# Kernel tuning notes

Measured on AMD Instinct MI355X. Metric: run time of the kernel, lower is better.

The kernel has to match this reference:

```python
import jax, jax.numpy as jnp
import numpy as np

EPS = 1e-8  # torch nn.CosineSimilarity default eps


def setup_inputs() -> dict:
    key = jax.random.key(0)
    k1, k2 = jax.random.split(key)
    text_encodings = jax.random.normal(k1, (65536, 256), dtype=jnp.float32)
    label_encodings = jax.random.normal(k2, (1024, 256), dtype=jnp.float32)
    return {"text_encodings": text_encodings, "label_encodings": label_encodings}


def reference(text_encodings, label_encodings):
    # cosine_sim(x, y) = x.y / max(||x||*||y||, eps), computed as one matmul
    dots = jnp.einsum('nd,ld->nl', text_encodings, label_encodings)  # [N, L]
    tn = jnp.linalg.norm(text_encodings, axis=-1)    # [N]
    ln = jnp.linalg.norm(label_encodings, axis=-1)   # [L]
    denom = jnp.maximum(tn[:, None] * ln[None, :], EPS)
    return dots / denom
```

## Files before the change

### kernel.cpp

```cpp
#include <hip/hip_runtime.h>
#include <hip/hip_bf16.h>

#define NT 65536
#define NL 1024
#define DD 256

#define BM 128
#define BN 128
#define BK 64
#define TPB 16

typedef __attribute__((ext_vector_type(4))) float f32x4;
typedef __attribute__((ext_vector_type(8))) short bf16x8;

__device__ inline short f2bf(float x) {
    union { __hip_bfloat16 b; short s; } u;
    u.b = __float2bfloat16(x);
    return u.s;
}

__device__ inline void gload_lds16(const void* g, void* l) {
    __builtin_amdgcn_global_load_lds((const __attribute__((address_space(1))) void*)g,
                                     (__attribute__((address_space(3))) void*)l,
                                     16, 0, 0);
}

__global__ __launch_bounds__(256) void prep_k(const float* __restrict__ A,
                                              const float* __restrict__ Bm,
                                              short* __restrict__ Abf,
                                              short* __restrict__ Bbf,
                                              float* __restrict__ rt,
                                              float* __restrict__ rl) {
    int gw   = (blockIdx.x * 256 + threadIdx.x) >> 6;
    int lane = threadIdx.x & 63;
    if (gw >= NT + NL) return;
    const float* src = (gw < NT) ? (A + (size_t)gw * DD) : (Bm + (size_t)(gw - NT) * DD);
    short*       dst = (gw < NT) ? (Abf + (size_t)gw * DD) : (Bbf + (size_t)(gw - NT) * DD);
    float4 v = reinterpret_cast<const float4*>(src)[lane];
    short4 o;
    o.x = f2bf(v.x); o.y = f2bf(v.y); o.z = f2bf(v.z); o.w = f2bf(v.w);
    reinterpret_cast<short4*>(dst)[lane] = o;
    float s = v.x * v.x + v.y * v.y + v.z * v.z + v.w * v.w;
#pragma unroll
    for (int off = 32; off > 0; off >>= 1) s += __shfl_xor(s, off);
    if (lane == 0) {
        float r = 1.0f / fmaxf(sqrtf(s), 1e-20f);
        if (gw < NT) rt[gw] = r; else rl[gw - NT] = r;
    }
}

__global__ __launch_bounds__(512, 2) void cosim_bf_k(const short* __restrict__ Abf,
                                                     const short* __restrict__ Bbf,
                                                     const float* __restrict__ rt,
                                                     const float* __restrict__ rl,
                                                     float* __restrict__ C) {
    __shared__ short Bs[BN * DD];
    __shared__ short As[4][BM * BK];
    __shared__ float rnA[TPB * BM];
    __shared__ float rnB[BN];

    const int tid  = threadIdx.x;
    const int lane = tid & 63;
    const int w    = tid >> 6;
    const int wr   = w >> 2;
    const int wc   = w & 3;

    const int xcd   = blockIdx.x & 7;
    const int g2    = blockIdx.x >> 3;
    const int bx    = g2 & 7;
    const int sub   = g2 >> 3;
    const int strip = xcd * 4 + sub;
    const int m0b   = strip * (TPB * BM);
    const int l0    = bx * BN;

    {
        const int r2 = lane >> 5;
        const int ch = lane & 31;
#pragma unroll
        for (int i = 0; i < 8; ++i) {
            int rbase = w * 16 + i * 2;
            int row   = rbase + r2;
            int cg    = ch ^ (row & 7);
            gload_lds16(Bbf + (size_t)(l0 + row) * DD + cg * 8, &Bs[rbase * DD]);
        }
    }
#pragma unroll
    for (int i = 0; i < 4; ++i) {
        int r = tid + i * 512;
        rnA[r] = rt[m0b + r];
    }
    if (tid < BN) rnB[tid] = rl[l0 + tid];
    __syncthreads();

    const int r8  = lane >> 3;
    const int ch8 = lane & 7;
    const int cg8 = ch8 ^ r8;
    auto stageA = [&](int g) {
        const short* base = Abf + (size_t)(m0b + (g >> 2) * BM) * DD + (g & 3) * BK;
        short* dst = As[g & 3];
#pragma unroll
        for (int i = 0; i < 2; ++i) {
            int rbase = w * 16 + i * 8;
            gload_lds16(base + (size_t)(rbase + r8) * DD + cg8 * 8, &dst[rbase * BK]);
        }
    };

    stageA(0);
    stageA(1);

    const int fr = lane & 15;
    const int fq = lane >> 4;
    const int cc = lane & 15;

#pragma unroll 1
    for (int t = 0; t < TPB; ++t) {
        f32x4 acc[4][2] = {};
#pragma unroll
        for (int kt = 0; kt < 4; ++kt) {
            const int g = t * 4 + kt;
            if (kt == 0) {
                stageA(g + 2);
                if (t == 0) asm volatile("s_waitcnt vmcnt(4)" ::: "memory");
                else        asm volatile("s_waitcnt vmcnt(36)" ::: "memory");
            } else if (kt == 1) {
                stageA(g + 2);
                if (t == 0) asm volatile("s_waitcnt vmcnt(4)" ::: "memory");
                else        asm volatile("s_waitcnt vmcnt(34)" ::: "memory");
            } else if (kt == 2) {
                if (t < TPB - 1) { stageA(g + 2); asm volatile("s_waitcnt vmcnt(4)" ::: "memory"); }
                else             { asm volatile("s_waitcnt vmcnt(2)" ::: "memory"); }
            } else {
                if (t < TPB - 1) { stageA(g + 2); asm volatile("s_waitcnt vmcnt(4)" ::: "memory"); }
                else             { asm volatile("s_waitcnt vmcnt(0)" ::: "memory"); }
            }
            __builtin_amdgcn_s_barrier();

            const short* A_ = As[g & 3];
#pragma unroll
            for (int ks = 0; ks < 2; ++ks) {
                bf16x8 af[4], bf2[2];
#pragma unroll
                for (int i = 0; i < 4; ++i) {
                    int row = wr * 64 + i * 16 + fr;
                    int ck  = (ks * 4 + fq) ^ (row & 7);
                    af[i] = *reinterpret_cast<const bf16x8*>(&A_[row * BK + ck * 8]);
                }
#pragma unroll
                for (int j = 0; j < 2; ++j) {
                    int row = wc * 32 + j * 16 + fr;
                    int c   = kt * 8 + ks * 4 + fq;
                    int ck  = c ^ (row & 7);
                    bf2[j] = *reinterpret_cast<const bf16x8*>(&Bs[row * DD + ck * 8]);
                }
#pragma unroll
                for (int i = 0; i < 4; ++i)
#pragma unroll
                    for (int j = 0; j < 2; ++j)
                        acc[i][j] = __builtin_amdgcn_mfma_f32_16x16x32_bf16(
                            af[i], bf2[j], acc[i][j], 0, 0, 0);
            }
        }

        const int m0 = m0b + t * BM;
#pragma unroll
        for (int i = 0; i < 4; ++i) {
#pragma unroll
            for (int rr = 0; rr < 4; ++rr) {
                int lr = wr * 64 + i * 16 + fq * 4 + rr;
                float rs = rnA[t * BM + lr];
                float* crow = C + (size_t)(m0 + lr) * NL + l0;
#pragma unroll
                for (int j = 0; j < 2; ++j) {
                    int lc = wc * 32 + j * 16 + cc;
                    __builtin_nontemporal_store(acc[i][j][rr] * rs * rnB[lc], &crow[lc]);
                }
            }
        }
    }
}

__global__ __launch_bounds__(256) void norms_k(const float* __restrict__ A,
                                               const float* __restrict__ Bm,
                                               float* __restrict__ rt,
                                               float* __restrict__ rl) {
    int gw   = (blockIdx.x * 256 + threadIdx.x) >> 6;
    int lane = threadIdx.x & 63;
    if (gw >= NT + NL) return;
    const float* src = (gw < NT) ? (A + (size_t)gw * DD) : (Bm + (size_t)(gw - NT) * DD);
    float4 v = reinterpret_cast<const float4*>(src)[lane];
    float s = v.x * v.x + v.y * v.y + v.z * v.z + v.w * v.w;
#pragma unroll
    for (int off = 32; off > 0; off >>= 1) s += __shfl_xor(s, off);
    if (lane == 0) {
        float r = 1.0f / fmaxf(sqrtf(s), 1e-20f);
        if (gw < NT) rt[gw] = r; else rl[gw - NT] = r;
    }
}

__global__ __launch_bounds__(256, 2) void cosim_fused_k(const float* __restrict__ A,
                                                        const float* __restrict__ Bm,
                                                        const float* __restrict__ rt,
                                                        const float* __restrict__ rl,
                                                        float* __restrict__ C) {
    __shared__ short As[BM * BK];
    __shared__ short Bs[BN * BK];
    const int tid  = threadIdx.x;
    const int lane = tid & 63;
    const int wid  = tid >> 6;
    const int wr   = wid >> 1;
    const int wc   = wid & 1;
    const int orig = blockIdx.x;
    const int id   = (orig & 7) * (4096 / 8) + (orig >> 3);
    const int bx   = id & 7;
    const int by   = id >> 3;
    const int m0 = by * BM;
    const int l0 = bx * BN;
    const int srow = tid >> 4;
    const int sc4  = tid & 15;
    f32x4 ra[8], rb[8];
    auto loadg = [&](int kt) {
        const float* pa = A  + (size_t)m0 * DD + kt * BK;
        const float* pb = Bm + (size_t)l0 * DD + kt * BK;
#pragma unroll
        for (int i = 0; i < 8; ++i) {
            int row = srow + i * 16;
            ra[i] = reinterpret_cast<const f32x4*>(pa + (size_t)row * DD)[sc4];
            rb[i] = reinterpret_cast<const f32x4*>(pb + (size_t)row * DD)[sc4];
        }
    };
    auto stash = [&]() {
#pragma unroll
        for (int i = 0; i < 8; ++i) {
            int row = srow + i * 16;
            short4 pa, pb;
            pa.x = f2bf(ra[i].x); pa.y = f2bf(ra[i].y);
            pa.z = f2bf(ra[i].z); pa.w = f2bf(ra[i].w);
            pb.x = f2bf(rb[i].x); pb.y = f2bf(rb[i].y);
            pb.z = f2bf(rb[i].z); pb.w = f2bf(rb[i].w);
            *reinterpret_cast<short4*>(&As[row * BK + sc4 * 4]) = pa;
            *reinterpret_cast<short4*>(&Bs[row * BK + sc4 * 4]) = pb;
        }
    };
    f32x4 acc[4][4] = {};
    loadg(0);
#pragma unroll
    for (int kt = 0; kt < DD / BK; ++kt) {
        __syncthreads();
        stash();
        __syncthreads();
        if (kt < DD / BK - 1) loadg(kt + 1);
#pragma unroll
        for (int ks = 0; ks < 2; ++ks) {
            bf16x8 af[4], bfr[4];
            const int kof = ks * 32 + (lane >> 4) * 8;
            const int ar  = wr * 64 + (lane & 15);
            const int bc  = wc * 64 + (lane & 15);
#pragma unroll
            for (int i = 0; i < 4; ++i)
                af[i] = *reinterpret_cast<const bf16x8*>(&As[(ar + i * 16) * BK + kof]);
#pragma unroll
            for (int j = 0; j < 4; ++j)
                bfr[j] = *reinterpret_cast<const bf16x8*>(&Bs[(bc + j * 16) * BK + kof]);
#pragma unroll
            for (int i = 0; i < 4; ++i)
#pragma unroll
                for (int j = 0; j < 4; ++j)
                    acc[i][j] = __builtin_amdgcn_mfma_f32_16x16x32_bf16(
                        af[i], bfr[j], acc[i][j], 0, 0, 0);
        }
    }
    const int crow0 = m0 + wr * 64;
    const int ccol0 = l0 + wc * 64;
    const int rq = lane >> 4;
    const int cc = lane & 15;
#pragma unroll
    for (int i = 0; i < 4; ++i) {
#pragma unroll
        for (int r = 0; r < 4; ++r) {
            int row = crow0 + i * 16 + rq * 4 + r;
            float rsc = rt[row];
            float* crow = C + (size_t)row * NL;
#pragma unroll
            for (int j = 0; j < 4; ++j) {
                int col = ccol0 + j * 16 + cc;
                crow[col] = acc[i][j][r] * rsc * rl[col];
            }
        }
    }
}

extern "C" void kernel_launch(void* const* d_in, const int* in_sizes, int n_in,
                              void* d_out, int out_size, void* d_ws, size_t ws_size,
                              hipStream_t stream) {
    const float* A  = (const float*)d_in[0];
    const float* Bm = (const float*)d_in[1];
    float* C = (float*)d_out;

    const size_t abf_elems = (size_t)NT * DD;
    const size_t bbf_elems = (size_t)NL * DD;
    const size_t need = (abf_elems + bbf_elems) * sizeof(short)
                      + (NT + NL) * sizeof(float);

    if (ws_size >= need) {
        short* Abf = (short*)d_ws;
        short* Bbf = Abf + abf_elems;
        float* rt  = (float*)(Bbf + bbf_elems);
        float* rl  = rt + NT;
        prep_k<<<(NT + NL) / 4, 256, 0, stream>>>(A, Bm, Abf, Bbf, rt, rl);
        cosim_bf_k<<<256, 512, 0, stream>>>(Abf, Bbf, rt, rl, C);
    } else {
        float* rt = (float*)d_ws;
        float* rl = rt + NT;
        norms_k<<<(NT + NL) / 4, 256, 0, stream>>>(A, Bm, rt, rl);
        cosim_fused_k<<<(NL / BN) * (NT / BM), 256, 0, stream>>>(A, Bm, rt, rl, C);
    }
}
```

Before: 316.1 us.

## Deepen A-tile LDS pipeline to five buffers and use nontemporal loads in prep

The bf16 GEMM kernel's A-tile staging ring grows from four to five LDS buffers, so four tiles are kept in flight instead of two. Staging now happens after the barrier, and the vmcnt waits are retuned to match the deeper prefetch. The prep kernel reads its fp32 inputs with nontemporal loads to limit cache pollution. The extra buffer raises LDS use per block, which could hurt occupancy under the 2-blocks-per-CU launch bound, and the hand-tuned wait counts are fragile.

```diff
diff --git a/kernel.cpp b/kernel.cpp
--- a/kernel.cpp
+++ b/kernel.cpp
@@ -36,11 +36,11 @@
     if (gw >= NT + NL) return;
     const float* src = (gw < NT) ? (A + (size_t)gw * DD) : (Bm + (size_t)(gw - NT) * DD);
     short*       dst = (gw < NT) ? (Abf + (size_t)gw * DD) : (Bbf + (size_t)(gw - NT) * DD);
-    float4 v = reinterpret_cast<const float4*>(src)[lane];
+    f32x4 v = __builtin_nontemporal_load(reinterpret_cast<const f32x4*>(src) + lane);
     short4 o;
-    o.x = f2bf(v.x); o.y = f2bf(v.y); o.z = f2bf(v.z); o.w = f2bf(v.w);
+    o.x = f2bf(v[0]); o.y = f2bf(v[1]); o.z = f2bf(v[2]); o.w = f2bf(v[3]);
     reinterpret_cast<short4*>(dst)[lane] = o;
-    float s = v.x * v.x + v.y * v.y + v.z * v.z + v.w * v.w;
+    float s = v[0]*v[0] + v[1]*v[1] + v[2]*v[2] + v[3]*v[3];
 #pragma unroll
     for (int off = 32; off > 0; off >>= 1) s += __shfl_xor(s, off);
     if (lane == 0) {
@@ -55,7 +55,7 @@
                                                      const float* __restrict__ rl,
                                                      float* __restrict__ C) {
     __shared__ short Bs[BN * DD];
-    __shared__ short As[4][BM * BK];
+    __shared__ short As[5][BM * BK];
     __shared__ float rnA[TPB * BM];
     __shared__ float rnB[BN];
 
@@ -95,9 +95,9 @@
     const int r8  = lane >> 3;
     const int ch8 = lane & 7;
     const int cg8 = ch8 ^ r8;
-    auto stageA = [&](int g) {
+    auto stageA = [&](int g, int buf) {
         const short* base = Abf + (size_t)(m0b + (g >> 2) * BM) * DD + (g & 3) * BK;
-        short* dst = As[g & 3];
+        short* dst = As[buf];
 #pragma unroll
         for (int i = 0; i < 2; ++i) {
             int rbase = w * 16 + i * 8;
@@ -105,8 +105,9 @@
         }
     };
 
-    stageA(0);
-    stageA(1);
+    stageA(0, 0); stageA(1, 1); stageA(2, 2); stageA(3, 3);
+    int bread  = 0;
+    int bstage = 4;
 
     const int fr = lane & 15;
     const int fq = lane >> 4;
@@ -118,24 +119,23 @@
 #pragma unroll
         for (int kt = 0; kt < 4; ++kt) {
             const int g = t * 4 + kt;
-            if (kt == 0) {
-                stageA(g + 2);
-                if (t == 0) asm volatile("s_waitcnt vmcnt(4)" ::: "memory");
-                else        asm volatile("s_waitcnt vmcnt(36)" ::: "memory");
-            } else if (kt == 1) {
-                stageA(g + 2);
-                if (t == 0) asm volatile("s_waitcnt vmcnt(4)" ::: "memory");
-                else        asm volatile("s_waitcnt vmcnt(34)" ::: "memory");
-            } else if (kt == 2) {
-                if (t < TPB - 1) { stageA(g + 2); asm volatile("s_waitcnt vmcnt(4)" ::: "memory"); }
-                else             { asm volatile("s_waitcnt vmcnt(2)" ::: "memory"); }
+            if (t == 0) {
+                asm volatile("s_waitcnt vmcnt(6)" ::: "memory");
+            } else if (t == TPB - 1) {
+                if      (kt == 0) asm volatile("s_waitcnt vmcnt(38)" ::: "memory");
+                else if (kt == 1) asm volatile("s_waitcnt vmcnt(36)" ::: "memory");
+                else if (kt == 2) asm volatile("s_waitcnt vmcnt(34)" ::: "memory");
+                else              asm volatile("s_waitcnt vmcnt(32)" ::: "memory");
             } else {
-                if (t < TPB - 1) { stageA(g + 2); asm volatile("s_waitcnt vmcnt(4)" ::: "memory"); }
-                else             { asm volatile("s_waitcnt vmcnt(0)" ::: "memory"); }
+                asm volatile("s_waitcnt vmcnt(38)" ::: "memory");
             }
             __builtin_amdgcn_s_barrier();
 
-            const short* A_ = As[g & 3];
+            if (t < TPB - 1) stageA(g + 4, bstage);
+            bstage = (bstage == 4) ? 0 : bstage + 1;
+
+            const short* A_ = As[bread];
+            bread = (bread == 4) ? 0 : bread + 1;
 #pragma unroll
             for (int ks = 0; ks < 2; ++ks) {
                 bf16x8 af[4], bf2[2];
@@ -233,10 +233,10 @@
         for (int i = 0; i < 8; ++i) {
             int row = srow + i * 16;
             short4 pa, pb;
-            pa.x = f2bf(ra[i].x); pa.y = f2bf(ra[i].y);
-            pa.z = f2bf(ra[i].z); pa.w = f2bf(ra[i].w);
-            pb.x = f2bf(rb[i].x); pb.y = f2bf(rb[i].y);
-            pb.z = f2bf(rb[i].z); pb.w = f2bf(rb[i].w);
+            pa.x = f2bf(ra[i][0]); pa.y = f2bf(ra[i][1]);
+            pa.z = f2bf(ra[i][2]); pa.w = f2bf(ra[i][3]);
+            pb.x = f2bf(rb[i][0]); pb.y = f2bf(rb[i][1]);
+            pb.z = f2bf(rb[i][2]); pb.w = f2bf(rb[i][3]);
             *reinterpret_cast<short4*>(&As[row * BK + sc4 * 4]) = pa;
             *reinterpret_cast<short4*>(&Bs[row * BK + sc4 * 4]) = pb;
         }
```

Result: slower. 336.9 us (+6.6%).
